# Optimization experiments

Hardware: AMD Instinct MI355X
Metric: run time of the kernel (lower is better)

Reference implementation:

```python
import jax, jax.numpy as jnp
import numpy as np
from jax import lax

B, T, K = 8192, 512, 5


def setup_inputs() -> dict:
    key = jax.random.key(0)
    k1, k2, k3, k4 = jax.random.split(key, 4)
    potentials = jax.random.normal(k1, (B, T, K), dtype=jnp.float32)
    transition_params = jax.random.normal(k2, (K, K), dtype=jnp.float32) * 0.1
    sequence_lengths = jax.random.randint(k3, (B,), 1, T + 1, dtype=jnp.int32)
    tag_indices = jax.random.randint(k4, (B, T), 0, K, dtype=jnp.int32)
    return {
        "potentials": potentials,
        "transition_params": transition_params,
        "sequence_lengths": sequence_lengths,
        "tag_indices": tag_indices,
    }


def _crf(potentials, transition_params, sequence_lengths, tag_indices):
    Bn, Tn, Kn = potentials.shape
    alpha0 = potentials[:, 0]                        # (B, K)
    pots_rest = jnp.swapaxes(potentials[:, 1:], 0, 1)  # (T-1, B, K)
    ts = jnp.arange(1, Tn)
    valid = ts[:, None] < sequence_lengths[None, :]    # (T-1, B)
    tag_range = jnp.arange(Kn, dtype=jnp.int32)

    # ---- Viterbi forward: max-product DP with backpointers ----
    def vit_step(alpha, inp):
        pot_t, v = inp
        scores = alpha[:, :, None] + transition_params[None]  # (B, K, K) over prev i -> next j
        bp = jnp.argmax(scores, axis=1).astype(jnp.int32)     # (B, K)
        new_alpha = jnp.max(scores, axis=1) + pot_t
        alpha = jnp.where(v[:, None], new_alpha, alpha)       # freeze past seq end
        bp = jnp.where(v[:, None], bp, tag_range[None])       # identity bp past seq end
        return alpha, bp

    alpha_v, bps = lax.scan(vit_step, alpha0, (pots_rest, valid))
    last_tag = jnp.argmax(alpha_v, axis=1).astype(jnp.int32)  # (B,)

    # ---- backtrack ----
    def back_step(tag, bp_t):
        prev = jnp.take_along_axis(bp_t, tag[:, None], axis=1)[:, 0]
        return prev, prev

    _, prev_tags = lax.scan(back_step, last_tag, bps, reverse=True)  # (T-1, B) tags 0..T-2
    decoded = jnp.concatenate([jnp.swapaxes(prev_tags, 0, 1), last_tag[:, None]], axis=1)
    mask = jnp.arange(Tn)[None] < sequence_lengths[:, None]          # (B, T)
    decoded = jnp.where(mask, decoded, 0)

    # ---- forward algorithm: log partition ----
    def fwd_step(alpha, inp):
        pot_t, v = inp
        new_alpha = jax.nn.logsumexp(alpha[:, :, None] + transition_params[None], axis=1) + pot_t
        return jnp.where(v[:, None], new_alpha, alpha), None

    alpha_f, _ = lax.scan(fwd_step, alpha0, (pots_rest, valid))
    log_norm = jax.nn.logsumexp(alpha_f, axis=1)                     # (B,)

    # ---- gold sequence score ----
    unary = jnp.take_along_axis(potentials, tag_indices[:, :, None], axis=2)[:, :, 0]  # (B, T)
    unary = jnp.sum(jnp.where(mask, unary, 0.0), axis=1)
    trans_sc = transition_params[tag_indices[:, :-1], tag_indices[:, 1:]]              # (B, T-1)
    tmask = jnp.arange(1, Tn)[None] < sequence_lengths[:, None]
    binary = jnp.sum(jnp.where(tmask, trans_sc, 0.0), axis=1)

    log_likelihood = unary + binary - log_norm
    return decoded, log_likelihood


def reference(potentials, transition_params, sequence_lengths, tag_indices):
    return _crf(potentials, transition_params, sequence_lengths, tag_indices)
```

## Files before the change

kernel.cpp:

```cpp
#include <hip/hip_runtime.h>
#include <stdint.h>

#define KK 5
#define TT 512

template<int P> __device__ __forceinline__ float swzf(float v) {
  return __int_as_float(__builtin_amdgcn_ds_swizzle(__float_as_int(v), P));
}
template<int P> __device__ __forceinline__ int swzi(int v) {
  return __builtin_amdgcn_ds_swizzle(v, P);
}
#define BC0 0x018
#define BC1 0x038
#define BC2 0x058
#define BC3 0x078
#define BC4 0x098
#define X1 0x041F
#define X2 0x081F
#define X4 0x101F

__device__ __forceinline__ float sel5f(float v0,float v1,float v2,float v3,float v4,int ct){
  float u=v0; u=(ct==1)?v1:u; u=(ct==2)?v2:u; u=(ct==3)?v3:u; u=(ct==4)?v4:u; return u;
}
__device__ __forceinline__ uint32_t sel5u(uint32_t w0,uint32_t w1,uint32_t w2,uint32_t w3,uint32_t w4,int ct){
  uint32_t u=w0; u=(ct==1)?w1:u; u=(ct==2)?w2:u; u=(ct==3)?w3:u; u=(ct==4)?w4:u; return u;
}
__device__ __forceinline__ int telt(const int4 (&tp)[2], int s) {
  const int4 v = (s < 4) ? tp[0] : tp[1];
  const int m = s & 3;
  return m == 0 ? v.x : (m == 1 ? v.y : (m == 2 ? v.z : v.w));
}

__device__ __forceinline__ void loadCol(float (&d)[8], const float* __restrict__ colp, int k) {
  const int t0 = k * 8 + 1;
  if (k < TT / 8 - 1) {
#pragma unroll
    for (int s = 0; s < 8; ++s) d[s] = colp[(t0 + s) * KK];
  } else {
#pragma unroll
    for (int s = 0; s < 8; ++s) d[s] = colp[min(t0 + s, TT - 1) * KK];
  }
}
__device__ __forceinline__ void loadTag(int4 (&tp)[2], const int* __restrict__ tg, int k) {
  tp[0] = *(const int4*)(tg + 8 * k);
  tp[1] = *(const int4*)(tg + 8 * k + 4);
}

__device__ __forceinline__ void vit_map_block(const float (&pv)[8], int k, int len_eff,
                                              const float (&trc)[KK], float& a,
                                              int jj, int g, int r,
                                              uint32_t* __restrict__ s_map) {
  uint32_t bits = 0;
#pragma unroll
  for (int s = 0; s < 8; ++s) {
    const float av0 = swzf<BC0>(a), av1 = swzf<BC1>(a), av2 = swzf<BC2>(a),
                av3 = swzf<BC3>(a), av4 = swzf<BC4>(a);
    const float s0 = av0 + trc[0], s1 = av1 + trc[1], s2 = av2 + trc[2],
                s3 = av3 + trc[3], s4 = av4 + trc[4];
    const float bm = fmaxf(fmaxf(fmaxf(s0, s1), fmaxf(s2, s3)), s4);
    int bi = 4;
    bi = (s3 == bm) ? 3 : bi;
    bi = (s2 == bm) ? 2 : bi;
    bi = (s1 == bm) ? 1 : bi;
    bi = (s0 == bm) ? 0 : bi;
    const int t = k * 8 + s + 1;
    const bool act = (t < len_eff);
    a = act ? (bm + pv[s]) : a;
    const int bie = act ? bi : jj;
    bits |= (uint32_t)bie << (3 * s);
  }
  const uint32_t w0 = (uint32_t)__builtin_amdgcn_ds_bpermute(((g << 3) + 0) << 2, (int)bits);
  const uint32_t w1 = (uint32_t)__builtin_amdgcn_ds_bpermute(((g << 3) + 1) << 2, (int)bits);
  const uint32_t w2 = (uint32_t)__builtin_amdgcn_ds_bpermute(((g << 3) + 2) << 2, (int)bits);
  const uint32_t w3 = (uint32_t)__builtin_amdgcn_ds_bpermute(((g << 3) + 3) << 2, (int)bits);
  const uint32_t w4 = (uint32_t)__builtin_amdgcn_ds_bpermute(((g << 3) + 4) << 2, (int)bits);
  int cur = jj;
  uint32_t dec = 0;
#pragma unroll
  for (int s = 7; s >= 0; --s) {
    const uint32_t w = sel5u(w0, w1, w2, w3, w4, cur);
    const int b3 = (int)((w >> (3 * s)) & 7u);
    dec |= (uint32_t)b3 << (3 * s);
    cur = b3;
  }
  if (r < 5) s_map[g * 321 + k * 5 + jj] = dec;
}

__device__ __forceinline__ void fwd_blk(const float (&pv)[8], const int4 (&tp)[2],
                                        int k, int len, int len_eff,
                                        const float (&Wc)[KK], const float (&trcR)[KK],
                                        float& p, float& Cacc,
                                        float& pvcar, int& tagcar,
                                        float& usum, float& bsum, int r) {
#pragma unroll
  for (int s = 0; s < 8; ++s) {
    const float p0 = swzf<BC0>(p), p1 = swzf<BC1>(p), p2 = swzf<BC2>(p),
                p3 = swzf<BC3>(p), p4 = swzf<BC4>(p);
    const float u  = fmaf(p1, Wc[1], p0 * Wc[0]);
    const float v2 = fmaf(p3, Wc[3], p2 * Wc[2]);
    const float acc = fmaf(p4, Wc[4], u + v2);
    const float E = __expf(pv[s]);
    const int t = k * 8 + s + 1;
    const bool act = (t < len_eff);
    p = act ? (acc * E) : p;
  }
#pragma unroll
  for (int s2 = 0; s2 < 8; ++s2) {
    const int t = k * 8 + s2;
    const int ct = telt(tp, s2);
    const int pt = (s2 == 0) ? tagcar : telt(tp, s2 - 1);
    const float potv = (s2 == 0) ? pvcar : pv[s2 - 1];
    const bool um = (t < len) && (ct == r);
    usum += um ? potv : 0.0f;
    bsum += (um && t >= 1) ? sel5f(trcR[0], trcR[1], trcR[2], trcR[3], trcR[4], pt) : 0.0f;
  }
  pvcar = pv[7];
  tagcar = telt(tp, 7);
  float m = p;
  m = fmaxf(m, swzf<X1>(m));
  m = fmaxf(m, swzf<X2>(m));
  m = fmaxf(m, swzf<X4>(m));
  p *= (1.0f / m);
  Cacc += __logf(m);
}

__launch_bounds__(64)
__global__ void crf_kernel(const float* __restrict__ pot,
                           const float* __restrict__ trans,
                           const int* __restrict__ lens,
                           const int* __restrict__ tags,
                           float* __restrict__ out,
                           int B, int T) {
  __shared__ uint32_t s_map[8 * 321];
  __shared__ uint32_t s_chosen[8 * 65];
  const int lane = threadIdx.x;
  const int g = lane >> 3, r = lane & 7;
  const int jj = (r < 5) ? r : 4;
  const unsigned u = blockIdx.x;
  const int role = (u >> 3) & 1;
  const int idx = (int)((u & 7u) | ((u >> 4) << 3));
  const int b = idx * 8 + g;
  const int len = lens[b];
  const int len_eff = (r < 5) ? len : 0;
  const float* __restrict__ prow = pot + (size_t)b * (T * KK);
  const float* __restrict__ colp = prow + jj;

  int ml = len;
  ml = max(ml, __shfl_xor(ml, 8));
  ml = max(ml, __shfl_xor(ml, 16));
  ml = max(ml, __shfl_xor(ml, 32));
  const int nblk = (ml + 7) >> 3;

  if (role == 0) {
    float trc[KK];
#pragma unroll
    for (int i = 0; i < KK; ++i) trc[i] = trans[i * KK + jj];
    float a = (r < 5) ? prow[jj] : -3.0e38f;

    float pA[8], pB[8], pC[8];
    loadCol(pA, colp, 0);
    loadCol(pB, colp, min(1, nblk - 1));
    loadCol(pC, colp, min(2, nblk - 1));
    int blk = 0;
    while (true) {
      vit_map_block(pA, blk, len_eff, trc, a, jj, g, r, s_map);
      if (++blk == nblk) break;
      loadCol(pA, colp, min(blk + 2, nblk - 1));
      vit_map_block(pB, blk, len_eff, trc, a, jj, g, r, s_map);
      if (++blk == nblk) break;
      loadCol(pB, colp, min(blk + 2, nblk - 1));
      vit_map_block(pC, blk, len_eff, trc, a, jj, g, r, s_map);
      if (++blk == nblk) break;
      loadCol(pC, colp, min(blk + 2, nblk - 1));
    }
    float bm = a;
    bm = fmaxf(bm, swzf<X1>(bm));
    bm = fmaxf(bm, swzf<X2>(bm));
    bm = fmaxf(bm, swzf<X4>(bm));
    int cand = (r < 5 && a == bm) ? r : 7;
    cand = min(cand, swzi<X1>(cand));
    cand = min(cand, swzi<X2>(cand));
    cand = min(cand, swzi<X4>(cand));
    const int last = cand;

    if (r == 0) {
      int tag = last;
      for (int k2 = nblk - 1; k2 >= 0; --k2) {
        const uint32_t w = s_map[g * 321 + k2 * 5 + tag];
        s_chosen[g * 65 + k2] = w;
        tag = (int)(w & 7u);
      }
    }

    float* __restrict__ orow = out + (size_t)b * T;
#pragma unroll
    for (int kk = 0; kk < 8; ++kk) {
      const int k2 = kk * 8 + r;
      const uint32_t w = s_chosen[g * 65 + k2];
      const int base = k2 * 8;
      float f[8];
#pragma unroll
      for (int pI = 0; pI < 8; ++pI)
        f[pI] = (base + pI < len) ? (float)((w >> (3 * pI)) & 7u) : 0.0f;
      *(float4*)(orow + base)     = make_float4(f[0], f[1], f[2], f[3]);
      *(float4*)(orow + base + 4) = make_float4(f[4], f[5], f[6], f[7]);
    }

  } else {
    float Wc[KK], trcR[KK];
#pragma unroll
    for (int i = 0; i < KK; ++i) {
      trcR[i] = trans[i * KK + jj];
      Wc[i] = __expf(trcR[i]);
    }
    const float pj0 = prow[jj];
    float p = (r < 5) ? __expf(pj0) : 0.0f;
    float Cacc = 0.0f;
    float usum = 0.0f, bsum = 0.0f;
    float pvcar = pj0;
    int tagcar = 0;
    const int* __restrict__ tg = tags + (size_t)b * T;

    float pA[8], pB[8], pC[8];
    int4 TA[2], TB[2], TC[2];
    loadCol(pA, colp, 0);                loadTag(TA, tg, 0);
    loadCol(pB, colp, min(1, nblk - 1)); loadTag(TB, tg, min(1, nblk - 1));
    loadCol(pC, colp, min(2, nblk - 1)); loadTag(TC, tg, min(2, nblk - 1));
    int blk = 0;
    while (true) {
      fwd_blk(pA, TA, blk, len, len_eff, Wc, trcR, p, Cacc, pvcar, tagcar, usum, bsum, r);
      if (++blk == nblk) break;
      loadCol(pA, colp, min(blk + 2, nblk - 1)); loadTag(TA, tg, min(blk + 2, nblk - 1));
      fwd_blk(pB, TB, blk, len, len_eff, Wc, trcR, p, Cacc, pvcar, tagcar, usum, bsum, r);
      if (++blk == nblk) break;
      loadCol(pB, colp, min(blk + 2, nblk - 1)); loadTag(TB, tg, min(blk + 2, nblk - 1));
      fwd_blk(pC, TC, blk, len, len_eff, Wc, trcR, p, Cacc, pvcar, tagcar, usum, bsum, r);
      if (++blk == nblk) break;
      loadCol(pC, colp, min(blk + 2, nblk - 1)); loadTag(TC, tg, min(blk + 2, nblk - 1));
    }
    float sc = usum + bsum;
    sc += swzf<X1>(sc);
    sc += swzf<X2>(sc);
    sc += swzf<X4>(sc);
    float ps = p;
    ps += swzf<X1>(ps);
    ps += swzf<X2>(ps);
    ps += swzf<X4>(ps);
    const float logZ = Cacc + __logf(ps);
    if (r == 0) out[(size_t)B * T + b] = sc - logZ;
  }
}

extern "C" void kernel_launch(void* const* d_in, const int* in_sizes, int n_in,
                              void* d_out, int out_size, void* d_ws, size_t ws_size,
                              hipStream_t stream) {
  const float* pot   = (const float*)d_in[0];
  const float* trans = (const float*)d_in[1];
  const int*   lens  = (const int*)d_in[2];
  const int*   tags  = (const int*)d_in[3];
  float* out = (float*)d_out;

  const int B = in_sizes[2];
  const int T = in_sizes[3] / B;

  const int nblocks = 2 * (B / 8);
  crf_kernel<<<nblocks, 64, 0, stream>>>(pot, trans, lens, tags, out, B, T);
}
```

Baseline: 88.98 us.

## Sort sequences by length so each block groups similar-length sequences

Adds a counting-sort pre-pass kernel that orders batch indices by sequence length into workspace, and the CRF kernel indexes sequences through this order. Since each block of 8 sequences iterates up to the longest length in its group, grouping similar lengths removes padded timesteps. The cost is an extra kernel launch and single-block sort, plus non-contiguous sequence assignment.

```diff
diff --git a/kernel.cpp b/kernel.cpp
--- a/kernel.cpp
+++ b/kernel.cpp
@@ -44,6 +44,44 @@
 __device__ __forceinline__ void loadTag(int4 (&tp)[2], const int* __restrict__ tg, int k) {
   tp[0] = *(const int4*)(tg + 8 * k);
   tp[1] = *(const int4*)(tg + 8 * k + 4);
+}
+
+__global__ void sort_by_len(const int* __restrict__ lens, int* __restrict__ order, int B) {
+  __shared__ int hist[513];
+  __shared__ int off[513];
+  const int tid = threadIdx.x;
+  for (int i = tid; i < 513; i += 1024) hist[i] = 0;
+  __syncthreads();
+  for (int b = tid; b < B; b += 1024) atomicAdd(&hist[lens[b]], 1);
+  __syncthreads();
+  if (tid < 64) {
+    int local[9];
+    int sum = 0;
+#pragma unroll
+    for (int j = 0; j < 9; ++j) {
+      const int i = tid * 9 + j;
+      const int v = (i < 513) ? hist[i] : 0;
+      local[j] = sum;
+      sum += v;
+    }
+    int inc = sum;
+#pragma unroll
+    for (int d = 1; d < 64; d <<= 1) {
+      const int n = __shfl_up(inc, d);
+      inc += (tid >= d) ? n : 0;
+    }
+    const int excl = inc - sum;
+#pragma unroll
+    for (int j = 0; j < 9; ++j) {
+      const int i = tid * 9 + j;
+      if (i < 513) off[i] = excl + local[j];
+    }
+  }
+  __syncthreads();
+  for (int b = tid; b < B; b += 1024) {
+    const int p = atomicAdd(&off[lens[b]], 1);
+    order[p] = b;
+  }
 }
 
 __device__ __forceinline__ void vit_map_block(const float (&pv)[8], int k, int len_eff,
@@ -129,6 +167,7 @@
                            const float* __restrict__ trans,
                            const int* __restrict__ lens,
                            const int* __restrict__ tags,
+                           const int* __restrict__ order,
                            float* __restrict__ out,
                            int B, int T) {
   __shared__ uint32_t s_map[8 * 321];
@@ -139,7 +178,7 @@
   const unsigned u = blockIdx.x;
   const int role = (u >> 3) & 1;
   const int idx = (int)((u & 7u) | ((u >> 4) << 3));
-  const int b = idx * 8 + g;
+  const int b = order[idx * 8 + g];
   const int len = lens[b];
   const int len_eff = (r < 5) ? len : 0;
   const float* __restrict__ prow = pot + (size_t)b * (T * KK);
@@ -263,6 +302,10 @@
   const int B = in_sizes[2];
   const int T = in_sizes[3] / B;
 
+  int* order = (int*)d_ws;
+
+  sort_by_len<<<1, 1024, 0, stream>>>(lens, order, B);
+
   const int nblocks = 2 * (B / 8);
-  crf_kernel<<<nblocks, 64, 0, stream>>>(pot, trans, lens, tags, out, B, T);
-}
+  crf_kernel<<<nblocks, 64, 0, stream>>>(pot, trans, lens, tags, order, out, B, T);
+}
```

After: 94.08 us. 5.7% more time.
